# Kernel tuning notes

Hardware: AMD Instinct MI355X
Metric: run time of the kernel (lower is better)

Reference implementation:

```python
import jax, jax.numpy as jnp
import numpy as np

HEAD_DIM = 64  # hidden_dim 1024 // heads_num 16


def setup_inputs() -> dict:
    key = jax.random.key(0)
    ks = jax.random.split(key, 5)
    B, S, H = 2, 4096, 1024
    std = 1.0 / np.sqrt(H)
    return {
        "x": jax.random.normal(ks[0], (B, S, H), jnp.float32),
        "Wq": jax.random.normal(ks[1], (H, H), jnp.float32) * std,
        "bq": jnp.zeros((H,), jnp.float32),
        "Wk": jax.random.normal(ks[2], (H, H), jnp.float32) * std,
        "bk": jnp.zeros((H,), jnp.float32),
        "Wv": jax.random.normal(ks[3], (H, H), jnp.float32) * std,
        "bv": jnp.zeros((H,), jnp.float32),
        "Wo": jax.random.normal(ks[4], (H, H), jnp.float32) * std,
        "bo": jnp.zeros((H,), jnp.float32),
    }


def reference(x, Wq, bq, Wk, bk, Wv, bv, Wo, bo):
    # Linear projections (torch Linear: x @ W^T + b)
    q = jnp.einsum("bsh,oh->bso", x, Wq) + bq
    k = jnp.einsum("bsh,oh->bso", x, Wk) + bk
    v = jnp.einsum("bsh,oh->bso", x, Wv) + bv
    # all_to_all is identity on a single device (world size 1)
    scale = jnp.float32(HEAD_DIM) ** 0.5
    # Faithful to source: attention over the FULL hidden dim (no head split),
    # full [B, S, S] score matrix.
    scores = jnp.einsum("bqh,bkh->bqk", q, k) / scale
    weights = jax.nn.softmax(scores, axis=-1)
    attn = jnp.einsum("bqk,bkh->bqh", weights, v)
    out = jnp.einsum("bsh,oh->bso", attn, Wo) + bo
    return out
```

## Files before the change

### kernel.cpp

```cpp
#include <hip/hip_runtime.h>
#include <stdint.h>


typedef __bf16 bf16x8 __attribute__((ext_vector_type(8)));
typedef float  f32x4  __attribute__((ext_vector_type(4)));

__device__ __forceinline__ unsigned short f32_to_bf16_rne(float f) {
    uint32_t u = __builtin_bit_cast(uint32_t, f);
    uint32_t r = (u + 0x7FFFu + ((u >> 16) & 1u)) >> 16;
    return (unsigned short)r;
}

#define BM 128
#define BN 128
#define BK 64

__global__ __launch_bounds__(256) void cvt_all(
    const float* __restrict__ x,
    const float* __restrict__ w0, const float* __restrict__ w1,
    const float* __restrict__ w2, const float* __restrict__ w3,
    unsigned short* __restrict__ x16, unsigned short* __restrict__ w16,
    float* __restrict__ rsum)
{
    int b = blockIdx.x;
    if (b < 8192) {
        int i = (b * 256 + threadIdx.x) * 4;
        float4 v = *(const float4*)(x + i);
        ushort4 o;
        o.x = f32_to_bf16_rne(v.x);
        o.y = f32_to_bf16_rne(v.y);
        o.z = f32_to_bf16_rne(v.z);
        o.w = f32_to_bf16_rne(v.w);
        *(ushort4*)(x16 + i) = o;
    } else if (b < 8192 + 4096) {
        int bb = b - 8192;
        int which = bb >> 10;
        const float* src = which == 0 ? w0 : which == 1 ? w1 : which == 2 ? w2 : w3;
        int i = ((bb & 1023) * 256 + threadIdx.x) * 4;
        float4 v = *(const float4*)(src + i);
        ushort4 o;
        o.x = f32_to_bf16_rne(v.x);
        o.y = f32_to_bf16_rne(v.y);
        o.z = f32_to_bf16_rne(v.z);
        o.w = f32_to_bf16_rne(v.w);
        *(ushort4*)(w16 + (size_t)which * 1048576 + i) = o;
    } else {
        int i = ((b - 8192 - 4096) * 256 + threadIdx.x) * 4;
        *(float4*)(rsum + i) = float4{0.f, 0.f, 0.f, 0.f};
    }
}

template <int KC>
__device__ __forceinline__ void gemm_core(
    const unsigned short* __restrict__ Ab,
    const unsigned short* __restrict__ Bb,
    unsigned short* ldsA, unsigned short* ldsB,
    int mBase, int nBase, int lane, int wave, f32x4 (&acc)[4][4])
{
    const int quad = lane >> 4;
    const int l16  = lane & 15;
    const int wr   = wave >> 1;
    const int wc   = wave & 1;

    for (int k0 = 0; k0 < KC; k0 += BK) {
        #pragma unroll
        for (int i = 0; i < 4; ++i) {
            int base = (i * 4 + wave) * 64;
            int s    = base + lane;
            int row  = s >> 3;
            int col  = ((s ^ (s >> 3)) & 7) * 8;
            __builtin_amdgcn_global_load_lds(
                (const __attribute__((address_space(1))) void*)(Ab + (size_t)(mBase + row) * KC + (size_t)(k0 + col)),
                (__attribute__((address_space(3))) void*)(&ldsA[base * 8]),
                16, 0, 0);
        }
        #pragma unroll
        for (int i = 0; i < 4; ++i) {
            int base = (i * 4 + wave) * 64;
            int s    = base + lane;
            int row  = s >> 3;
            int col  = ((s ^ (s >> 3)) & 7) * 8;
            __builtin_amdgcn_global_load_lds(
                (const __attribute__((address_space(1))) void*)(Bb + (size_t)(nBase + row) * KC + (size_t)(k0 + col)),
                (__attribute__((address_space(3))) void*)(&ldsB[base * 8]),
                16, 0, 0);
        }
        __syncthreads();

        #pragma unroll
        for (int kk = 0; kk < 2; ++kk) {
            bf16x8 af[4], bfv[4];
            #pragma unroll
            for (int mi = 0; mi < 4; ++mi) {
                int r = wr * 64 + mi * 16 + l16;
                int c = kk * 4 + quad;
                af[mi] = *(const bf16x8*)(&ldsA[r * BK + (((c ^ r) & 7) << 3)]);
            }
            #pragma unroll
            for (int ni = 0; ni < 4; ++ni) {
                int r = wc * 64 + ni * 16 + l16;
                int c = kk * 4 + quad;
                bfv[ni] = *(const bf16x8*)(&ldsB[r * BK + (((c ^ r) & 7) << 3)]);
            }
            #pragma unroll
            for (int mi = 0; mi < 4; ++mi)
                #pragma unroll
                for (int ni = 0; ni < 4; ++ni)
                    acc[mi][ni] = __builtin_amdgcn_mfma_f32_16x16x32_bf16(
                        af[mi], bfv[ni], acc[mi][ni], 0, 0, 0);
        }
        __syncthreads();
    }
}

template <int MODE, int KC>
__global__ __launch_bounds__(256) void gemm_bt(
    const unsigned short* __restrict__ A,
    const unsigned short* __restrict__ Bt,
    void* __restrict__ C, void* __restrict__ C2,
    const float* __restrict__ b0, const float* __restrict__ b1,
    const float* __restrict__ b2, const float* __restrict__ rowsum,
    int M, int N, long long aZ, long long bZ, long long cZ)
{
    __shared__ unsigned short ldsA[BM * BK];
    __shared__ unsigned short ldsB[BN * BK];

    int G  = gridDim.x * gridDim.y * gridDim.z;
    int l  = blockIdx.x + gridDim.x * (blockIdx.y + gridDim.y * blockIdx.z);
    int perx = G >> 3;
    int idx  = (l & 7) * perx + (l >> 3);
    int NB = gridDim.x, Z = gridDim.z;
    int mb = idx / (NB * Z);
    int rem = idx - mb * (NB * Z);
    int zb = rem / NB;
    int nb = rem - zb * NB;

    const unsigned short* Ab = A  + (size_t)zb * aZ;
    const unsigned short* Bb = Bt + (size_t)zb * bZ;

    const int tid  = threadIdx.x;
    const int lane = tid & 63;
    const int wave = tid >> 6;
    const int quad = lane >> 4;
    const int l16  = lane & 15;
    const int wr   = wave >> 1;
    const int wc   = wave & 1;
    const int mBase = mb * BM;
    const int nBase = nb * BN;

    f32x4 acc[4][4] = {};
    gemm_core<KC>(Ab, Bb, ldsA, ldsB, mBase, nBase, lane, wave, acc);

    if (MODE == 5) {
        const float* bias = (zb == 0) ? b0 : (zb == 1) ? b1 : b2;
        unsigned short* Cz = (zb < 2) ? ((unsigned short*)C + (size_t)zb * cZ)
                                      : (unsigned short*)C2;
        #pragma unroll
        for (int mi = 0; mi < 4; ++mi)
            #pragma unroll
            for (int ni = 0; ni < 4; ++ni) {
                int col = nBase + wc * 64 + ni * 16 + l16;
                float b = bias[col];
                #pragma unroll
                for (int r = 0; r < 4; ++r) {
                    int row = mBase + wr * 64 + mi * 16 + quad * 4 + r;
                    Cz[(size_t)row * N + col] = f32_to_bf16_rne(acc[mi][ni][r] + b);
                }
            }
    } else {
        float* Cz = (float*)C + (size_t)zb * cZ;
        const float* rs = rowsum + (size_t)zb * M;
        #pragma unroll
        for (int mi = 0; mi < 4; ++mi) {
            #pragma unroll
            for (int r = 0; r < 4; ++r) {
                int row = mBase + wr * 64 + mi * 16 + quad * 4 + r;
                float inv = 1.f / rs[row];
                #pragma unroll
                for (int ni = 0; ni < 4; ++ni) {
                    int col = nBase + wc * 64 + ni * 16 + l16;
                    Cz[(size_t)row * N + col] = acc[mi][ni][r] * inv + b0[col];
                }
            }
        }
    }
}

__global__ __launch_bounds__(256) void gemm_dual(
    const unsigned short* __restrict__ wo,
    const unsigned short* __restrict__ v16,
    unsigned short* __restrict__ vot16,
    const unsigned short* __restrict__ q16,
    const unsigned short* __restrict__ k16,
    unsigned short* __restrict__ p16,
    float* __restrict__ rowsum)
{
    __shared__ unsigned short ldsA[BM * BK];
    __shared__ unsigned short ldsB[BN * BK];

    const int S = 4096, H = 1024;
    const long long SH = (long long)S * H;

    int l   = blockIdx.x;
    int idx = (l & 7) * 320 + (l >> 3);

    const unsigned short* Ab;
    const unsigned short* Bb;
    unsigned short* Cb;
    float* rs = nullptr;
    int mBase, nBase;
    bool isScore;

    if (idx < 512) {
        int z = idx >> 8, m = (idx >> 5) & 7, n = idx & 31;
        Ab = wo;
        Bb = v16 + (size_t)z * SH;
        Cb = vot16 + (size_t)z * SH;
        mBase = m * BM; nBase = n * BN;
        isScore = false;
    } else {
        int sid = idx - 512;
        int m = sid >> 6, z = (sid >> 5) & 1, n = sid & 31;
        Ab = q16 + (size_t)z * SH;
        Bb = k16 + (size_t)z * SH;
        Cb = p16 + (size_t)z * S * S;
        rs = rowsum + (size_t)z * S;
        mBase = m * BM; nBase = n * BN;
        isScore = true;
    }

    const int tid  = threadIdx.x;
    const int lane = tid & 63;
    const int wave = tid >> 6;
    const int quad = lane >> 4;
    const int l16  = lane & 15;
    const int wr   = wave >> 1;
    const int wc   = wave & 1;

    f32x4 acc[4][4] = {};
    gemm_core<1024>(Ab, Bb, ldsA, ldsB, mBase, nBase, lane, wave, acc);

    if (isScore) {
        #pragma unroll
        for (int mi = 0; mi < 4; ++mi) {
            #pragma unroll
            for (int r = 0; r < 4; ++r) {
                int row = mBase + wr * 64 + mi * 16 + quad * 4 + r;
                float e[4];
                float partial = 0.f;
                #pragma unroll
                for (int ni = 0; ni < 4; ++ni) {
                    e[ni] = __expf(acc[mi][ni][r] * 0.125f);
                    partial += e[ni];
                }
                #pragma unroll
                for (int ni = 0; ni < 4; ++ni) {
                    int col = nBase + wc * 64 + ni * 16 + l16;
                    Cb[(size_t)row * 4096 + col] = f32_to_bf16_rne(e[ni]);
                }
                #pragma unroll
                for (int off = 1; off < 16; off <<= 1)
                    partial += __shfl_xor(partial, off, 64);
                if (l16 == 0) atomicAdd(&rs[row], partial);
            }
        }
    } else {
        #pragma unroll
        for (int mi = 0; mi < 4; ++mi)
            #pragma unroll
            for (int ni = 0; ni < 4; ++ni) {
                int col = nBase + wc * 64 + ni * 16 + l16;
                #pragma unroll
                for (int r = 0; r < 4; ++r) {
                    int row = mBase + wr * 64 + mi * 16 + quad * 4 + r;
                    Cb[(size_t)row * 4096 + col] = f32_to_bf16_rne(acc[mi][ni][r]);
                }
            }
    }
}

extern "C" void kernel_launch(void* const* d_in, const int* in_sizes, int n_in,
                              void* d_out, int out_size, void* d_ws, size_t ws_size,
                              hipStream_t stream)
{
    const float* x  = (const float*)d_in[0];
    const float* Wq = (const float*)d_in[1];
    const float* bq = (const float*)d_in[2];
    const float* Wk = (const float*)d_in[3];
    const float* bk = (const float*)d_in[4];
    const float* Wv = (const float*)d_in[5];
    const float* bv = (const float*)d_in[6];
    const float* Wo = (const float*)d_in[7];
    const float* bo = (const float*)d_in[8];
    float* out = (float*)d_out;

    const int Bsz = 2, S = 4096, H = 1024;
    const int M = Bsz * S;

    char* p = (char*)d_ws;
    auto alloc = [&](size_t bytes) -> char* {
        char* r = p; p += (bytes + 255) & ~(size_t)255; return r;
    };
    unsigned short* w16  = (unsigned short*)alloc((size_t)4 * H * H * 2);
    unsigned short* wq16 = w16;
    unsigned short* wo16 = w16 + (size_t)3 * H * H;
    unsigned short* q16  = (unsigned short*)alloc((size_t)M * H * 2);
    unsigned short* k16  = (unsigned short*)alloc((size_t)M * H * 2);
    unsigned short* v16  = (unsigned short*)alloc((size_t)M * H * 2);
    unsigned short* vot16= (unsigned short*)alloc((size_t)Bsz * H * S * 2);
    float*          rsum = (float*)alloc((size_t)Bsz * S * 4);
    char* region = alloc((size_t)Bsz * S * S * 2);
    unsigned short* x16 = (unsigned short*)region;
    unsigned short* p16 = (unsigned short*)region;

    cvt_all<<<8192 + 4096 + 8, 256, 0, stream>>>(x, Wq, Wk, Wv, Wo, x16, w16, rsum);

    gemm_bt<5, 1024><<<dim3(H / BN, M / BM, 3), 256, 0, stream>>>(
        x16, wq16, q16, v16, bq, bk, bv, nullptr, M, H,
        0, (long long)H * H, (long long)M * H);

    gemm_dual<<<2560, 256, 0, stream>>>(wo16, v16, vot16, q16, k16, p16, rsum);

    gemm_bt<6, 4096><<<dim3(H / BN, S / BM, 2), 256, 0, stream>>>(
        p16, vot16, out, nullptr, bo, nullptr, nullptr, rsum, S, H,
        (long long)S * S, (long long)H * S, (long long)S * H);
}
```

Measured before the change: 386.0 us.

## Fold Wv into Wo algebraically and compute V·Wo^T directly from x

The V projection and the Wo multiply are merged into one precomputed product F = Wo·Wv (H×H), built from a transposed bf16 copy of Wv made in the convert kernel. The transposed value matrix used by the final GEMM is then computed directly as F·x^T, which removes the full-size V projection GEMM. The V bias is folded into a final bias bv·Wo^T + bo that is computed in the convert kernel. The score GEMM moves out of the fused dual kernel into its own launch. The trade-off is one extra kernel launch, the loss of the previous score/vot fusion, and an extra bf16 rounding of the weight product F.

```diff
diff --git a/kernel.cpp b/kernel.cpp
--- a/kernel.cpp
+++ b/kernel.cpp
@@ -17,35 +17,72 @@
 
 __global__ __launch_bounds__(256) void cvt_all(
     const float* __restrict__ x,
-    const float* __restrict__ w0, const float* __restrict__ w1,
-    const float* __restrict__ w2, const float* __restrict__ w3,
+    const float* __restrict__ Wq, const float* __restrict__ Wk,
+    const float* __restrict__ Wo, const float* __restrict__ Wv,
+    const float* __restrict__ bv, const float* __restrict__ bo,
     unsigned short* __restrict__ x16, unsigned short* __restrict__ w16,
-    float* __restrict__ rsum)
-{
-    int b = blockIdx.x;
+    float* __restrict__ rsum, float* __restrict__ bfinal)
+{
+    const int b = blockIdx.x, tid = threadIdx.x;
     if (b < 8192) {
-        int i = (b * 256 + threadIdx.x) * 4;
+        int i = (b * 256 + tid) * 4;
         float4 v = *(const float4*)(x + i);
         ushort4 o;
-        o.x = f32_to_bf16_rne(v.x);
-        o.y = f32_to_bf16_rne(v.y);
-        o.z = f32_to_bf16_rne(v.z);
-        o.w = f32_to_bf16_rne(v.w);
+        o.x = f32_to_bf16_rne(v.x); o.y = f32_to_bf16_rne(v.y);
+        o.z = f32_to_bf16_rne(v.z); o.w = f32_to_bf16_rne(v.w);
         *(ushort4*)(x16 + i) = o;
-    } else if (b < 8192 + 4096) {
+    } else if (b < 11264) {
         int bb = b - 8192;
         int which = bb >> 10;
-        const float* src = which == 0 ? w0 : which == 1 ? w1 : which == 2 ? w2 : w3;
-        int i = ((bb & 1023) * 256 + threadIdx.x) * 4;
+        const float* src = which == 0 ? Wq : which == 1 ? Wk : Wo;
+        int i = ((bb & 1023) * 256 + tid) * 4;
         float4 v = *(const float4*)(src + i);
         ushort4 o;
-        o.x = f32_to_bf16_rne(v.x);
-        o.y = f32_to_bf16_rne(v.y);
-        o.z = f32_to_bf16_rne(v.z);
-        o.w = f32_to_bf16_rne(v.w);
+        o.x = f32_to_bf16_rne(v.x); o.y = f32_to_bf16_rne(v.y);
+        o.z = f32_to_bf16_rne(v.z); o.w = f32_to_bf16_rne(v.w);
         *(ushort4*)(w16 + (size_t)which * 1048576 + i) = o;
+    } else if (b < 11520) {
+        __shared__ unsigned short tl[64 * 68];
+        int t = b - 11264, tr = t >> 4, tc = t & 15;
+        #pragma unroll
+        for (int it = 0; it < 4; ++it) {
+            int r  = it * 16 + (tid >> 4);
+            int c0 = (tid & 15) * 4;
+            float4 v = *(const float4*)(Wv + (size_t)(tr * 64 + r) * 1024 + tc * 64 + c0);
+            tl[(c0 + 0) * 68 + r] = f32_to_bf16_rne(v.x);
+            tl[(c0 + 1) * 68 + r] = f32_to_bf16_rne(v.y);
+            tl[(c0 + 2) * 68 + r] = f32_to_bf16_rne(v.z);
+            tl[(c0 + 3) * 68 + r] = f32_to_bf16_rne(v.w);
+        }
+        __syncthreads();
+        #pragma unroll
+        for (int it = 0; it < 4; ++it) {
+            int c  = it * 16 + (tid >> 4);
+            int r0 = (tid & 15) * 4;
+            ushort4 o;
+            o.x = tl[c * 68 + r0 + 0]; o.y = tl[c * 68 + r0 + 1];
+            o.z = tl[c * 68 + r0 + 2]; o.w = tl[c * 68 + r0 + 3];
+            *(ushort4*)(w16 + (size_t)3 * 1048576 + (size_t)(tc * 64 + c) * 1024 + tr * 64 + r0) = o;
+        }
+    } else if (b < 11536) {
+        int bb = b - 11520;
+        int lane = tid & 63, wv_ = tid >> 6;
+        int rowBase = bb * 64 + wv_ * 16;
+        for (int rr = 0; rr < 16; ++rr) {
+            int row = rowBase + rr;
+            float partial = 0.f;
+            #pragma unroll
+            for (int t2 = 0; t2 < 16; ++t2) {
+                int h = t2 * 64 + lane;
+                partial += Wo[(size_t)row * 1024 + h] * bv[h];
+            }
+            #pragma unroll
+            for (int off = 32; off > 0; off >>= 1)
+                partial += __shfl_xor(partial, off, 64);
+            if (lane == 0) bfinal[row] = bo[row] + partial;
+        }
     } else {
-        int i = ((b - 8192 - 4096) * 256 + threadIdx.x) * 4;
+        int i = ((b - 11536) * 256 + tid) * 4;
         *(float4*)(rsum + i) = float4{0.f, 0.f, 0.f, 0.f};
     }
 }
@@ -117,10 +154,10 @@
 __global__ __launch_bounds__(256) void gemm_bt(
     const unsigned short* __restrict__ A,
     const unsigned short* __restrict__ Bt,
-    void* __restrict__ C, void* __restrict__ C2,
-    const float* __restrict__ b0, const float* __restrict__ b1,
-    const float* __restrict__ b2, const float* __restrict__ rowsum,
-    int M, int N, long long aZ, long long bZ, long long cZ)
+    void* __restrict__ C,
+    const float* __restrict__ b0, float* __restrict__ rowsum,
+    float alpha, int M, int N,
+    long long aZ, long long bZ, long long cZ)
 {
     __shared__ unsigned short ldsA[BM * BK];
     __shared__ unsigned short ldsB[BN * BK];
@@ -151,22 +188,46 @@
     f32x4 acc[4][4] = {};
     gemm_core<KC>(Ab, Bb, ldsA, ldsB, mBase, nBase, lane, wave, acc);
 
-    if (MODE == 5) {
-        const float* bias = (zb == 0) ? b0 : (zb == 1) ? b1 : b2;
-        unsigned short* Cz = (zb < 2) ? ((unsigned short*)C + (size_t)zb * cZ)
-                                      : (unsigned short*)C2;
+    if (MODE == 1) {
+        unsigned short* Cz = (unsigned short*)C + (size_t)zb * cZ;
         #pragma unroll
         for (int mi = 0; mi < 4; ++mi)
             #pragma unroll
             for (int ni = 0; ni < 4; ++ni) {
                 int col = nBase + wc * 64 + ni * 16 + l16;
-                float b = bias[col];
+                float b = b0 ? b0[col] : 0.f;
                 #pragma unroll
                 for (int r = 0; r < 4; ++r) {
                     int row = mBase + wr * 64 + mi * 16 + quad * 4 + r;
                     Cz[(size_t)row * N + col] = f32_to_bf16_rne(acc[mi][ni][r] + b);
                 }
             }
+    } else if (MODE == 3) {
+        unsigned short* Pz = (unsigned short*)C + (size_t)zb * cZ;
+        float* rs = rowsum + (size_t)zb * M;
+        #pragma unroll
+        for (int mi = 0; mi < 4; ++mi) {
+            #pragma unroll
+            for (int r = 0; r < 4; ++r) {
+                int row = mBase + wr * 64 + mi * 16 + quad * 4 + r;
+                float e[4];
+                float partial = 0.f;
+                #pragma unroll
+                for (int ni = 0; ni < 4; ++ni) {
+                    e[ni] = __expf(acc[mi][ni][r] * alpha);
+                    partial += e[ni];
+                }
+                #pragma unroll
+                for (int ni = 0; ni < 4; ++ni) {
+                    int col = nBase + wc * 64 + ni * 16 + l16;
+                    Pz[(size_t)row * N + col] = f32_to_bf16_rne(e[ni]);
+                }
+                #pragma unroll
+                for (int off = 1; off < 16; off <<= 1)
+                    partial += __shfl_xor(partial, off, 64);
+                if (l16 == 0) atomicAdd(&rs[row], partial);
+            }
+        }
     } else {
         float* Cz = (float*)C + (size_t)zb * cZ;
         const float* rs = rowsum + (size_t)zb * M;
@@ -186,47 +247,36 @@
     }
 }
 
-__global__ __launch_bounds__(256) void gemm_dual(
-    const unsigned short* __restrict__ wo,
-    const unsigned short* __restrict__ v16,
-    unsigned short* __restrict__ vot16,
-    const unsigned short* __restrict__ q16,
-    const unsigned short* __restrict__ k16,
-    unsigned short* __restrict__ p16,
-    float* __restrict__ rowsum)
+__global__ __launch_bounds__(256) void gemm_qkf(
+    const unsigned short* __restrict__ x16,
+    const unsigned short* __restrict__ w16,
+    unsigned short* __restrict__ q16,
+    unsigned short* __restrict__ k16,
+    unsigned short* __restrict__ F16,
+    const float* __restrict__ bq, const float* __restrict__ bk)
 {
     __shared__ unsigned short ldsA[BM * BK];
     __shared__ unsigned short ldsB[BN * BK];
 
-    const int S = 4096, H = 1024;
-    const long long SH = (long long)S * H;
-
     int l   = blockIdx.x;
-    int idx = (l & 7) * 320 + (l >> 3);
-
-    const unsigned short* Ab;
-    const unsigned short* Bb;
+    int idx = (l & 7) * 136 + (l >> 3);
+
+    const unsigned short *Ab, *Bb;
     unsigned short* Cb;
-    float* rs = nullptr;
+    const float* bias;
     int mBase, nBase;
-    bool isScore;
-
-    if (idx < 512) {
-        int z = idx >> 8, m = (idx >> 5) & 7, n = idx & 31;
-        Ab = wo;
-        Bb = v16 + (size_t)z * SH;
-        Cb = vot16 + (size_t)z * SH;
-        mBase = m * BM; nBase = n * BN;
-        isScore = false;
+    if (idx < 1024) {
+        int role = idx >> 9;
+        int s    = idx & 511;
+        mBase = (s >> 3) * BM; nBase = (s & 7) * BN;
+        Ab = x16; Bb = w16 + (size_t)role * 1048576;
+        Cb = role ? k16 : q16; bias = role ? bk : bq;
     } else {
-        int sid = idx - 512;
-        int m = sid >> 6, z = (sid >> 5) & 1, n = sid & 31;
-        Ab = q16 + (size_t)z * SH;
-        Bb = k16 + (size_t)z * SH;
-        Cb = p16 + (size_t)z * S * S;
-        rs = rowsum + (size_t)z * S;
-        mBase = m * BM; nBase = n * BN;
-        isScore = true;
+        int f = idx - 1024;
+        mBase = (f >> 3) * BM; nBase = (f & 7) * BN;
+        Ab = w16 + (size_t)2 * 1048576;
+        Bb = w16 + (size_t)3 * 1048576;
+        Cb = F16; bias = nullptr;
     }
 
     const int tid  = threadIdx.x;
@@ -240,43 +290,18 @@
     f32x4 acc[4][4] = {};
     gemm_core<1024>(Ab, Bb, ldsA, ldsB, mBase, nBase, lane, wave, acc);
 
-    if (isScore) {
-        #pragma unroll
-        for (int mi = 0; mi < 4; ++mi) {
+    #pragma unroll
+    for (int mi = 0; mi < 4; ++mi)
+        #pragma unroll
+        for (int ni = 0; ni < 4; ++ni) {
+            int col = nBase + wc * 64 + ni * 16 + l16;
+            float b = bias ? bias[col] : 0.f;
             #pragma unroll
             for (int r = 0; r < 4; ++r) {
                 int row = mBase + wr * 64 + mi * 16 + quad * 4 + r;
-                float e[4];
-                float partial = 0.f;
-                #pragma unroll
-                for (int ni = 0; ni < 4; ++ni) {
-                    e[ni] = __expf(acc[mi][ni][r] * 0.125f);
-                    partial += e[ni];
-                }
-                #pragma unroll
-                for (int ni = 0; ni < 4; ++ni) {
-                    int col = nBase + wc * 64 + ni * 16 + l16;
-                    Cb[(size_t)row * 4096 + col] = f32_to_bf16_rne(e[ni]);
-                }
-                #pragma unroll
-                for (int off = 1; off < 16; off <<= 1)
-                    partial += __shfl_xor(partial, off, 64);
-                if (l16 == 0) atomicAdd(&rs[row], partial);
-            }
-        }
-    } else {
-        #pragma unroll
-        for (int mi = 0; mi < 4; ++mi)
-            #pragma unroll
-            for (int ni = 0; ni < 4; ++ni) {
-                int col = nBase + wc * 64 + ni * 16 + l16;
-                #pragma unroll
-                for (int r = 0; r < 4; ++r) {
-                    int row = mBase + wr * 64 + mi * 16 + quad * 4 + r;
-                    Cb[(size_t)row * 4096 + col] = f32_to_bf16_rne(acc[mi][ni][r]);
-                }
-            }
-    }
+                Cb[(size_t)row * 1024 + col] = f32_to_bf16_rne(acc[mi][ni][r] + b);
+            }
+        }
 }
 
 extern "C" void kernel_launch(void* const* d_in, const int* in_sizes, int n_in,
@@ -294,7 +319,7 @@
     const float* bo = (const float*)d_in[8];
     float* out = (float*)d_out;
 
-    const int Bsz = 2, S = 4096, H = 1024;
+    const int S = 4096, H = 1024, Bsz = 2;
     const int M = Bsz * S;
 
     char* p = (char*)d_ws;
@@ -302,26 +327,30 @@
         char* r = p; p += (bytes + 255) & ~(size_t)255; return r;
     };
     unsigned short* w16  = (unsigned short*)alloc((size_t)4 * H * H * 2);
-    unsigned short* wq16 = w16;
-    unsigned short* wo16 = w16 + (size_t)3 * H * H;
+    unsigned short* F16  = (unsigned short*)alloc((size_t)H * H * 2);
     unsigned short* q16  = (unsigned short*)alloc((size_t)M * H * 2);
     unsigned short* k16  = (unsigned short*)alloc((size_t)M * H * 2);
-    unsigned short* v16  = (unsigned short*)alloc((size_t)M * H * 2);
     unsigned short* vot16= (unsigned short*)alloc((size_t)Bsz * H * S * 2);
-    float*          rsum = (float*)alloc((size_t)Bsz * S * 4);
+    float*          rsum = (float*)alloc((size_t)M * 4);
+    float*          bfin = (float*)alloc((size_t)H * 4);
     char* region = alloc((size_t)Bsz * S * S * 2);
     unsigned short* x16 = (unsigned short*)region;
     unsigned short* p16 = (unsigned short*)region;
 
-    cvt_all<<<8192 + 4096 + 8, 256, 0, stream>>>(x, Wq, Wk, Wv, Wo, x16, w16, rsum);
-
-    gemm_bt<5, 1024><<<dim3(H / BN, M / BM, 3), 256, 0, stream>>>(
-        x16, wq16, q16, v16, bq, bk, bv, nullptr, M, H,
-        0, (long long)H * H, (long long)M * H);
-
-    gemm_dual<<<2560, 256, 0, stream>>>(wo16, v16, vot16, q16, k16, p16, rsum);
+    cvt_all<<<11544, 256, 0, stream>>>(x, Wq, Wk, Wo, Wv, bv, bo,
+                                       x16, w16, rsum, bfin);
+
+    gemm_qkf<<<1088, 256, 0, stream>>>(x16, w16, q16, k16, F16, bq, bk);
+
+    gemm_bt<1, 1024><<<dim3(S / BN, H / BM, 2), 256, 0, stream>>>(
+        F16, x16, vot16, nullptr, nullptr, 1.f, H, S,
+        0, (long long)S * H, (long long)H * S);
+
+    gemm_bt<3, 1024><<<dim3(S / BN, S / BM, 2), 256, 0, stream>>>(
+        q16, k16, p16, nullptr, rsum, 0.125f, S, S,
+        (long long)S * H, (long long)S * H, (long long)S * S);
 
     gemm_bt<6, 4096><<<dim3(H / BN, S / BM, 2), 256, 0, stream>>>(
-        p16, vot16, out, nullptr, bo, nullptr, nullptr, rsum, S, H,
+        p16, vot16, out, bfin, rsum, 1.f, S, H,
         (long long)S * S, (long long)H * S, (long long)S * H);
 }
```

Measured after the change: 401.2 us. 3.9% more time.
